# Optimization experiments

Measured on AMD Instinct MI355X. Metric: run time of the kernel, lower is better.

Reference implementation:

```python
import jax, jax.numpy as jnp
import numpy as np

V, S, D, H, L, F = 32000, 1024, 1024, 16, 6, 4096
DH = D // H          # 64
HALF = DH // 2       # 32
EPS = 1e-5
ROPE_BASE = 10000.0


def setup_inputs() -> dict:
    key = jax.random.key(0)
    ks = jax.random.split(key, 16)
    std = 0.02
    inp = {
        "tokens": jax.random.randint(ks[0], (4, S), 0, V),
        "tok_emb": jax.random.normal(ks[1], (V, D), jnp.float32) * std,
        "ln1_s": jnp.ones((L, D), jnp.float32),
        "ln1_b": jnp.zeros((L, D), jnp.float32),
        "w_qkv": jax.random.normal(ks[2], (L, D, 3 * D), jnp.float32) * std,
        "w_proj": jax.random.normal(ks[3], (L, D, D), jnp.float32) * std,
        "ln2_s": jnp.ones((L, D), jnp.float32),
        "ln2_b": jnp.zeros((L, D), jnp.float32),
        "w_in": jax.random.normal(ks[4], (L, D, 2 * F), jnp.float32) * std,
        "w_out": jax.random.normal(ks[5], (L, F, D), jnp.float32) * std,
        "lnf_s": jnp.ones((D,), jnp.float32),
        "lnf_b": jnp.zeros((D,), jnp.float32),
        "w_score": jax.random.normal(ks[6], (D, 1), jnp.float32) * std,
        "w_cls": jax.random.normal(ks[7], (D, S), jnp.float32) * std,
    }
    return inp


def _layernorm(x, s, b):
    m = x.mean(-1, keepdims=True)
    v = ((x - m) ** 2).mean(-1, keepdims=True)
    return (x - m) * jax.lax.rsqrt(v + EPS) * s + b


def _rotate_half(x):
    x_even = x[..., ::2]
    x_odd = x[..., 1::2]
    return jnp.stack((-x_odd, x_even), axis=-1).reshape(x.shape)


def _rope_tables():
    inv_freq = 1.0 / (ROPE_BASE ** (jnp.arange(0, DH, 2, dtype=jnp.float32) / DH))
    pos = jnp.arange(S, dtype=jnp.float32)
    freqs = jnp.outer(pos, inv_freq)               # [S, DH/2]
    cos = jnp.repeat(jnp.cos(freqs), 2, axis=-1)   # [S, DH]
    sin = jnp.repeat(jnp.sin(freqs), 2, axis=-1)
    return cos, sin


def _forward(tokens, tok_emb, ln1_s, ln1_b, w_qkv, w_proj, ln2_s, ln2_b,
             w_in, w_out, lnf_s, lnf_b, w_score, w_cls):
    B = tokens.shape[0]
    cos, sin = _rope_tables()                      # [S, DH], broadcast over B,H
    lower = jnp.tril(jnp.ones((S, S), jnp.bool_))  # j <= i -> "down" subspace
    scale = HALF ** -0.5

    h = tok_emb[tokens]                            # [B, S, D]

    def block(h, p):
        l1s, l1b, Wqkv, Wp, l2s, l2b, Wi, Wo = p
        # --- dual-triangle attention ---
        qkv = _layernorm(h, l1s, l1b) @ Wqkv       # [B, S, 3D]
        q, k, v = jnp.split(qkv, 3, axis=-1)
        def heads(t):
            return t.reshape(B, S, H, DH).transpose(0, 2, 1, 3)  # [B,H,S,DH]
        q, k, v = heads(q), heads(k), heads(v)
        q = q * cos + _rotate_half(q) * sin
        k = k * cos + _rotate_half(k) * sin
        a_up = jnp.einsum('bhqd,bhkd->bhqk', q[..., :HALF], k[..., :HALF]) * scale
        a_dn = jnp.einsum('bhqd,bhkd->bhqk', q[..., HALF:], k[..., HALF:]) * scale
        logits = jnp.where(lower, a_dn, a_up)
        w = jax.nn.softmax(logits, axis=-1)
        o = jnp.einsum('bhqk,bhkd->bhqd', w, v)
        o = o.transpose(0, 2, 1, 3).reshape(B, S, D) @ Wp
        h = h + o
        # --- SwiGLU MLP ---
        g = _layernorm(h, l2s, l2b) @ Wi           # [B, S, 2F]
        a, b = jnp.split(g, 2, axis=-1)
        h = h + (jax.nn.silu(a) * b) @ Wo
        return h, None

    h, _ = jax.lax.scan(block, h, (ln1_s, ln1_b, w_qkv, w_proj, ln2_s, ln2_b, w_in, w_out))

    # pooling head: per-position scores -> softmax over positions -> weighted sum
    h = _layernorm(h, lnf_s, lnf_b)
    scores = h @ w_score                           # [B, S, 1]
    pw = jax.nn.softmax(scores, axis=1)
    pooled = jnp.sum(pw * h, axis=1)               # [B, D]
    return pooled @ w_cls                          # [B, S] logits over positions


def reference(tokens, tok_emb, ln1_s, ln1_b, w_qkv, w_proj, ln2_s, ln2_b,
              w_in, w_out, lnf_s, lnf_b, w_score, w_cls):
    return _forward(tokens, tok_emb, ln1_s, ln1_b, w_qkv, w_proj, ln2_s, ln2_b,
                    w_in, w_out, lnf_s, lnf_b, w_score, w_cls)
```

## Files before the change

### kernel.cpp

```cpp
#include <hip/hip_runtime.h>

#define Bsz 4
#define Ssz 1024
#define Dsz 1024
#define Hn  16
#define DHn 64
#define Ln  6
#define Fsz 4096
#define SCALE_ 0.1767766952966369f
#define LOG2E_ 1.4426950408889634f

typedef unsigned long long u64;
typedef __attribute__((ext_vector_type(8))) short bf16x8;
typedef __attribute__((ext_vector_type(4))) float f32x4;

__device__ __forceinline__ unsigned short f2bf(float f) {
  union { float f; unsigned int u; } v; v.f = f;
  unsigned int u = v.u + 0x7fffu + ((v.u >> 16) & 1u);
  return (unsigned short)(u >> 16);
}
__device__ __forceinline__ float bf2f(unsigned short h) {
  union { unsigned int u; float f; } v; v.u = ((unsigned int)h) << 16;
  return v.f;
}
__device__ __forceinline__ void gload_lds16(const void* g, void* lds) {
  __builtin_amdgcn_global_load_lds(
      (const __attribute__((address_space(1))) unsigned int*)g,
      (__attribute__((address_space(3))) unsigned int*)lds, 16, 0, 0);
}

__device__ __forceinline__ int swz_addr(int r, int lq) {
  int line = r >> 1;
  int u = ((r & 1) << 2) | lq;
  int s = u ^ (line & 7);
  return line * 128 + s * 16;
}

__global__ __launch_bounds__(256) void k_cossin(float* __restrict__ cosT, float* __restrict__ sinT) {
  int idx = blockIdx.x * 256 + threadIdx.x;
  if (idx >= Ssz * 32) return;
  int s = idx >> 5, i = idx & 31;
  float inv = powf(10000.f, -((float)(2 * i)) / 64.f);
  float f = (float)s * inv;
  cosT[idx] = cosf(f);
  sinT[idx] = sinf(f);
}

__global__ __launch_bounds__(256) void k_embed(const int* __restrict__ tokens,
                                               const float* __restrict__ emb,
                                               float* __restrict__ h) {
  int rs = blockIdx.x;
  int t = threadIdx.x;
  int tok = tokens[rs];
  *(float4*)&h[(u64)rs * Dsz + t * 4] = *(const float4*)&emb[(u64)tok * Dsz + t * 4];
}

template <int BF16OUT>
__global__ __launch_bounds__(256) void k_layernorm(const float* __restrict__ x,
                                                   const float* __restrict__ sc,
                                                   const float* __restrict__ bi,
                                                   void* outv) {
  int row = blockIdx.x, t = threadIdx.x;
  const float* xr = x + (u64)row * Dsz;
  float4 v = *(const float4*)&xr[t * 4];
  float sm = v.x + v.y + v.z + v.w;
  float sq = v.x * v.x + v.y * v.y + v.z * v.z + v.w * v.w;
#pragma unroll
  for (int m = 1; m < 64; m <<= 1) { sm += __shfl_xor(sm, m); sq += __shfl_xor(sq, m); }
  __shared__ float r1[4], r2[4];
  if ((t & 63) == 0) { r1[t >> 6] = sm; r2[t >> 6] = sq; }
  __syncthreads();
  sm = r1[0] + r1[1] + r1[2] + r1[3];
  sq = r2[0] + r2[1] + r2[2] + r2[3];
  float mean = sm * (1.f / Dsz);
  float inv = rsqrtf(sq * (1.f / Dsz) - mean * mean + 1e-5f);
  float4 s4 = *(const float4*)&sc[t * 4];
  float4 b4 = *(const float4*)&bi[t * 4];
  float y0 = (v.x - mean) * inv * s4.x + b4.x;
  float y1 = (v.y - mean) * inv * s4.y + b4.y;
  float y2 = (v.z - mean) * inv * s4.z + b4.z;
  float y3 = (v.w - mean) * inv * s4.w + b4.w;
  if (BF16OUT) {
    ushort4 o; o.x = f2bf(y0); o.y = f2bf(y1); o.z = f2bf(y2); o.w = f2bf(y3);
    *(ushort4*)((unsigned short*)outv + (u64)row * Dsz + t * 4) = o;
  } else {
    float4 o; o.x = y0; o.y = y1; o.z = y2; o.w = y3;
    *(float4*)((float*)outv + (u64)row * Dsz + t * 4) = o;
  }
}

__global__ __launch_bounds__(256) void k_wt(const float* __restrict__ in,
                                            unsigned short* __restrict__ out, int K, int N) {
  in += (u64)blockIdx.z * K * N;
  out += (u64)blockIdx.z * K * N;
  __shared__ float tile[32][33];
  int nb = blockIdx.x * 32, kb = blockIdx.y * 32;
  int t = threadIdx.x;
  int r = t >> 3, c4 = (t & 7) * 4;
  float4 v = *(const float4*)&in[(u64)(kb + r) * N + nb + c4];
  tile[r][c4] = v.x; tile[r][c4 + 1] = v.y; tile[r][c4 + 2] = v.z; tile[r][c4 + 3] = v.w;
  __syncthreads();
  ushort4 o;
  o.x = f2bf(tile[c4][r]); o.y = f2bf(tile[c4 + 1][r]);
  o.z = f2bf(tile[c4 + 2][r]); o.w = f2bf(tile[c4 + 3][r]);
  *(ushort4*)&out[(u64)(nb + r) * K + kb + c4] = o;
}

__global__ __launch_bounds__(256) void k_wt_pair(const float* __restrict__ in,
                                                 unsigned short* __restrict__ out) {
  in += (u64)blockIdx.z * Dsz * 2 * Fsz;
  out += (u64)blockIdx.z * 2 * Fsz * Dsz;
  __shared__ float tile[32][33];
  int nb = blockIdx.x * 32, kb = blockIdx.y * 32;
  int t = threadIdx.x;
  int r = t >> 3, c4 = (t & 7) * 4;
  int s0 = nb >> 1;
  int srccol = (c4 < 16) ? (s0 + c4) : (Fsz + s0 + (c4 - 16));
  float4 v = *(const float4*)&in[(u64)(kb + r) * (2 * Fsz) + srccol];
  tile[r][c4] = v.x; tile[r][c4 + 1] = v.y; tile[r][c4 + 2] = v.z; tile[r][c4 + 3] = v.w;
  __syncthreads();
  int sc = (r >> 1) + (r & 1) * 16;
  ushort4 o;
  o.x = f2bf(tile[c4][sc]); o.y = f2bf(tile[c4 + 1][sc]);
  o.z = f2bf(tile[c4 + 2][sc]); o.w = f2bf(tile[c4 + 3][sc]);
  *(ushort4*)&out[(u64)(nb + r) * Dsz + kb + c4] = o;
}

template <int EPI>
__global__ __launch_bounds__(256, 3)
void k_ring(const unsigned short* __restrict__ A,
            const unsigned short* __restrict__ Bt,
            const float* resid, void* Cout,
            int M, int N, int K, int KH) {
  __shared__ char lds[3][16384] __attribute__((aligned(16)));
  int t = threadIdx.x, w = t >> 6, l = t & 63;
  int wm = w >> 1, wn = w & 1;
  int lr = l & 15, lq = l >> 4;
  int bn = blockIdx.x, bm = blockIdx.y, kz = blockIdx.z;
  int NT = KH >> 5;
  int g0 = t, g1 = t + 256;
  int L0 = g0 >> 3, u0 = (g0 & 7) ^ (L0 & 7), row0 = 2 * L0 + (u0 >> 2), kc0 = (u0 & 3) * 8;
  int L1 = g1 >> 3, u1 = (g1 & 7) ^ (L1 & 7), row1 = 2 * L1 + (u1 >> 2), kc1 = (u1 & 3) * 8;
  const unsigned short* Az = A + (u64)kz * KH;
  const unsigned short* Bz = Bt + (u64)kz * KH;
  const char* Asrc0 = (const char*)(Az + (u64)(bm * 128 + row0) * K + kc0);
  const char* Asrc1 = (const char*)(Az + (u64)(bm * 128 + row1) * K + kc1);
  const char* Bsrc0 = (const char*)(Bz + (u64)(bn * 128 + row0) * K + kc0);
  const char* Bsrc1 = (const char*)(Bz + (u64)(bn * 128 + row1) * K + kc1);
  f32x4 acc[4][4];
#pragma unroll
  for (int i = 0; i < 4; ++i)
#pragma unroll
    for (int j = 0; j < 4; ++j) acc[i][j] = (f32x4){0.f, 0.f, 0.f, 0.f};
#define STG(slot, jj) { char* d_ = lds[slot]; \
    gload_lds16(Asrc0 + (u64)(jj) * 64, d_ + g0 * 16); \
    gload_lds16(Asrc1 + (u64)(jj) * 64, d_ + g1 * 16); \
    gload_lds16(Bsrc0 + (u64)(jj) * 64, d_ + 8192 + g0 * 16); \
    gload_lds16(Bsrc1 + (u64)(jj) * 64, d_ + 8192 + g1 * 16); }
  STG(0, 0); STG(1, 1);
  int cs = 0, ss = 2;
  for (int j = 0; j < NT; ++j) {
    if (j < NT - 1) asm volatile("s_waitcnt vmcnt(4)" ::: "memory");
    else            asm volatile("s_waitcnt vmcnt(0)" ::: "memory");
    __builtin_amdgcn_s_barrier();
    __builtin_amdgcn_sched_barrier(0);
    const char* Ab = lds[cs];
    const char* Bb = lds[cs] + 8192;
    if (j + 2 < NT) STG(ss, j + 2);
    bf16x8 afrag[4], bfrag[4];
#pragma unroll
    for (int ni = 0; ni < 4; ++ni)
      bfrag[ni] = *(const bf16x8*)(Bb + swz_addr(wn * 64 + ni * 16 + lr, lq));
#pragma unroll
    for (int mi = 0; mi < 4; ++mi)
      afrag[mi] = *(const bf16x8*)(Ab + swz_addr(wm * 64 + mi * 16 + lr, lq));
    __builtin_amdgcn_s_setprio(1);
#pragma unroll
    for (int mi = 0; mi < 4; ++mi)
#pragma unroll
      for (int ni = 0; ni < 4; ++ni)
        acc[mi][ni] = __builtin_amdgcn_mfma_f32_16x16x32_bf16(afrag[mi], bfrag[ni], acc[mi][ni], 0, 0, 0);
    __builtin_amdgcn_s_setprio(0);
    cs = (cs == 2) ? 0 : cs + 1;
    ss = (ss == 2) ? 0 : ss + 1;
  }
#undef STG
  u64 zoff = (u64)kz * M * N;
#pragma unroll
  for (int mi = 0; mi < 4; ++mi)
#pragma unroll
    for (int ni = 0; ni < 4; ++ni)
#pragma unroll
      for (int r = 0; r < 4; ++r) {
        int row = bm * 128 + wm * 64 + mi * 16 + lq * 4 + r;
        int col = bn * 128 + wn * 64 + ni * 16 + lr;
        float v = acc[mi][ni][r];
        if (EPI == 3) {
          float pv = __shfl_xor(v, 1);
          if ((lr & 1) == 0) {
            float res = v / (1.f + __expf(-v)) * pv;
            ((unsigned short*)Cout)[(u64)row * (N >> 1) + (col >> 1)] = f2bf(res);
          }
        } else {
          u64 idx = (u64)row * N + col;
          if (EPI == 0) ((float*)Cout)[zoff + idx] = v;
          else if (EPI == 1) ((unsigned short*)Cout)[idx] = f2bf(v);
          else ((float*)Cout)[idx] = resid[idx] + v;
        }
      }
}

__global__ __launch_bounds__(256) void k_redres(const float* __restrict__ p0,
                                                const float* __restrict__ p1,
                                                float* __restrict__ h) {
  u64 i = ((u64)blockIdx.x * 256 + threadIdx.x) * 4;
  float4 a = *(float4*)&h[i];
  float4 b = *(const float4*)&p0[i];
  float4 c = *(const float4*)&p1[i];
  a.x += b.x + c.x; a.y += b.y + c.y; a.z += b.z + c.z; a.w += b.w + c.w;
  *(float4*)&h[i] = a;
}

__global__ __launch_bounds__(256) void k_rope_heads(const unsigned short* __restrict__ qkv,
                                                    const float* __restrict__ cosT,
                                                    const float* __restrict__ sinT,
                                                    unsigned short* __restrict__ q_r,
                                                    unsigned short* __restrict__ k_r,
                                                    unsigned short* __restrict__ v_t) {
  int st = blockIdx.x, hh = blockIdx.y, b = blockIdx.z;
  int t = threadIdx.x;
  int r = t >> 2, cg = (t & 3) * 16;
  int s = st * 64 + r;
  u64 rowb = ((u64)(b * Ssz + s)) * (3 * Dsz);
  u64 bh = (u64)(b * Hn + hh);
  const unsigned int* qp = (const unsigned int*)(qkv + rowb + hh * 64 + cg);
  const unsigned int* kp = (const unsigned int*)(qkv + rowb + Dsz + hh * 64 + cg);
  const unsigned short* vp = qkv + rowb + 2 * Dsz + hh * 64 + cg;
  uint4 qv0 = *(const uint4*)qp, qv1 = *(const uint4*)(qp + 4);
  uint4 kv0 = *(const uint4*)kp, kv1 = *(const uint4*)(kp + 4);
  int i0 = s * 32 + (cg >> 1);
  float4 cA0 = *(const float4*)&cosT[i0], cA1 = *(const float4*)&cosT[i0 + 4];
  float4 sA0 = *(const float4*)&sinT[i0], sA1 = *(const float4*)&sinT[i0 + 4];
  unsigned int qw[8] = {qv0.x, qv0.y, qv0.z, qv0.w, qv1.x, qv1.y, qv1.z, qv1.w};
  unsigned int kw[8] = {kv0.x, kv0.y, kv0.z, kv0.w, kv1.x, kv1.y, kv1.z, kv1.w};
  float cA[8] = {cA0.x, cA0.y, cA0.z, cA0.w, cA1.x, cA1.y, cA1.z, cA1.w};
  float sA[8] = {sA0.x, sA0.y, sA0.z, sA0.w, sA1.x, sA1.y, sA1.z, sA1.w};
  unsigned int oq[8], ok[8];
#pragma unroll
  for (int j = 0; j < 8; ++j) {
    float c = cA[j], sn = sA[j];
    float qe = bf2f((unsigned short)(qw[j] & 0xffff)), qo = bf2f((unsigned short)(qw[j] >> 16));
    float ke = bf2f((unsigned short)(kw[j] & 0xffff)), ko = bf2f((unsigned short)(kw[j] >> 16));
    oq[j] = (unsigned int)f2bf(qe * c - qo * sn) | ((unsigned int)f2bf(qo * c + qe * sn) << 16);
    ok[j] = (unsigned int)f2bf(ke * c - ko * sn) | ((unsigned int)f2bf(ko * c + ke * sn) << 16);
  }
  u64 dst = (bh * Ssz + s) * 64 + cg;
  uint4 a0; a0.x = oq[0]; a0.y = oq[1]; a0.z = oq[2]; a0.w = oq[3];
  uint4 a1; a1.x = oq[4]; a1.y = oq[5]; a1.z = oq[6]; a1.w = oq[7];
  ((uint4*)&q_r[dst])[0] = a0; ((uint4*)&q_r[dst])[1] = a1;
  uint4 b0; b0.x = ok[0]; b0.y = ok[1]; b0.z = ok[2]; b0.w = ok[3];
  uint4 b1; b1.x = ok[4]; b1.y = ok[5]; b1.z = ok[6]; b1.w = ok[7];
  ((uint4*)&k_r[dst])[0] = b0; ((uint4*)&k_r[dst])[1] = b1;
  __shared__ unsigned short vt_lds[64][65];
  uint4 vv0 = *(const uint4*)vp, vv1 = *(const uint4*)(vp + 8);
  unsigned int vw[8] = {vv0.x, vv0.y, vv0.z, vv0.w, vv1.x, vv1.y, vv1.z, vv1.w};
#pragma unroll
  for (int j = 0; j < 8; ++j) {
    vt_lds[r][cg + 2 * j] = (unsigned short)(vw[j] & 0xffff);
    vt_lds[r][cg + 2 * j + 1] = (unsigned short)(vw[j] >> 16);
  }
  __syncthreads();
  unsigned int ov[8];
#pragma unroll
  for (int j = 0; j < 8; ++j) {
    unsigned short lo = vt_lds[cg + 2 * j][r], hi = vt_lds[cg + 2 * j + 1][r];
    ov[j] = (unsigned int)lo | ((unsigned int)hi << 16);
  }
  u64 vdst = bh * ((u64)DHn * Ssz) + (u64)r * Ssz + st * 64 + cg;
  uint4 c0v; c0v.x = ov[0]; c0v.y = ov[1]; c0v.z = ov[2]; c0v.w = ov[3];
  uint4 c1v; c1v.x = ov[4]; c1v.y = ov[5]; c1v.z = ov[6]; c1v.w = ov[7];
  ((uint4*)&v_t[vdst])[0] = c0v; ((uint4*)&v_t[vdst])[1] = c1v;
}

__global__ __launch_bounds__(256) void k_attn(const unsigned short* __restrict__ qr,
                                              const unsigned short* __restrict__ kr,
                                              const unsigned short* __restrict__ vt,
                                              unsigned short* __restrict__ outp) {
  __shared__ unsigned short Klds[2][2][64 * 32] __attribute__((aligned(16)));
  __shared__ unsigned short Vlds[2][2][64 * 32] __attribute__((aligned(16)));
  __shared__ unsigned short Plds[4][16 * 64] __attribute__((aligned(16)));
  int qt = blockIdx.x, hh = blockIdx.y, b = blockIdx.z;
  int t = threadIdx.x, w = t >> 6, l = t & 63;
  int lr = l & 15, lq = l >> 4;
  u64 bh = (u64)(b * Hn + hh);
  const unsigned short* Qp = qr + bh * (Ssz * DHn);
  const unsigned short* Kp = kr + bh * (Ssz * DHn);
  const unsigned short* Vp = vt + bh * ((u64)DHn * Ssz);
  int q0 = qt * 64 + w * 16;
  bf16x8 qlo = *(const bf16x8*)&Qp[(q0 + lr) * DHn + lq * 8];
  bf16x8 qhi = *(const bf16x8*)&Qp[(q0 + lr) * DHn + 32 + lq * 8];
  int srow = t >> 2;
  int scol8 = (t & 3) * 8;
#define STAGEKV(bufi, kbase)                                                         \
  do {                                                                               \
    gload_lds16(&Kp[((kbase) + srow) * 64 + scol8],      (char*)&Klds[bufi][0][0] + t * 16); \
    gload_lds16(&Kp[((kbase) + srow) * 64 + 32 + scol8], (char*)&Klds[bufi][1][0] + t * 16); \
    gload_lds16(&Vp[(u64)srow * Ssz + (kbase) + scol8],      (char*)&Vlds[bufi][0][0] + t * 16); \
    gload_lds16(&Vp[(u64)srow * Ssz + (kbase) + 32 + scol8], (char*)&Vlds[bufi][1][0] + t * 16); \
  } while (0)
  float m_col = -1e30f, lsum = 0.f;
  float m_row[4] = {-1e30f, -1e30f, -1e30f, -1e30f};
  f32x4 o[4];
#pragma unroll
  for (int r = 0; r < 4; ++r) o[r] = (f32x4){0.f, 0.f, 0.f, 0.f};
  char* Pw = (char*)&Plds[w][0];

  STAGEKV(0, 0);
  asm volatile("s_waitcnt vmcnt(0)" ::: "memory");
  __syncthreads();
  int buf = 0;
  const float lsc = SCALE_ * LOG2E_;
  for (int kb = 0; kb < Ssz; kb += 64) {
    if (kb + 64 < Ssz) STAGEKV(buf ^ 1, kb + 64);
    float p[4][4];
#pragma unroll
    for (int ct = 0; ct < 4; ++ct) {
      bf16x8 klo = *(const bf16x8*)&Klds[buf][0][(ct * 16 + lr) * 32 + lq * 8];
      bf16x8 khi = *(const bf16x8*)&Klds[buf][1][(ct * 16 + lr) * 32 + lq * 8];
      f32x4 z = (f32x4){0.f, 0.f, 0.f, 0.f};
      f32x4 slo = __builtin_amdgcn_mfma_f32_16x16x32_bf16(klo, qlo, z, 0, 0, 0);
      f32x4 shi = __builtin_amdgcn_mfma_f32_16x16x32_bf16(khi, qhi, z, 0, 0, 0);
      int kg0 = kb + ct * 16 + lq * 4;
      int qg = q0 + lr;
#pragma unroll
      for (int r = 0; r < 4; ++r) p[ct][r] = (kg0 + r <= qg ? shi[r] : slo[r]) * lsc;
    }
    float tm = p[0][0];
#pragma unroll
    for (int ct = 0; ct < 4; ++ct)
#pragma unroll
      for (int r = 0; r < 4; ++r) tm = fmaxf(tm, p[ct][r]);
    tm = fmaxf(tm, __shfl_xor(tm, 16));
    tm = fmaxf(tm, __shfl_xor(tm, 32));
    if (__any(tm > m_col)) {
      float m_new = fmaxf(m_col, tm);
      lsum *= exp2f(m_col - m_new);
      m_col = m_new;
#pragma unroll
      for (int r = 0; r < 4; ++r) {
        float mr = __shfl(m_col, lq * 4 + r);
        float scf = exp2f(m_row[r] - mr);
        m_row[r] = mr;
        o[0][r] *= scf; o[1][r] *= scf; o[2][r] *= scf; o[3][r] *= scf;
      }
    }
#pragma unroll
    for (int ct = 0; ct < 4; ++ct) {
      float e0 = exp2f(p[ct][0] - m_col);
      float e1 = exp2f(p[ct][1] - m_col);
      float e2 = exp2f(p[ct][2] - m_col);
      float e3 = exp2f(p[ct][3] - m_col);
      lsum += e0 + e1 + e2 + e3;
      ushort4 pk; pk.x = f2bf(e0); pk.y = f2bf(e1); pk.z = f2bf(e2); pk.w = f2bf(e3);
      int byte_ = (lr * 128 + ct * 32 + lq * 8) ^ ((lr & 7) << 4);
      *(ushort4*)(Pw + byte_) = pk;
    }
    asm volatile("s_waitcnt lgkmcnt(0)" ::: "memory");
    __builtin_amdgcn_sched_barrier(0);
#pragma unroll
    for (int ks = 0; ks < 2; ++ks) {
      int pb = (lr * 128 + ks * 64 + lq * 16) ^ ((lr & 7) << 4);
      bf16x8 pa = *(const bf16x8*)(Pw + pb);
#pragma unroll
      for (int nt = 0; nt < 4; ++nt) {
        bf16x8 vb = *(const bf16x8*)&Vlds[buf][ks][(nt * 16 + lr) * 32 + lq * 8];
        o[nt] = __builtin_amdgcn_mfma_f32_16x16x32_bf16(pa, vb, o[nt], 0, 0, 0);
      }
    }
    asm volatile("s_waitcnt vmcnt(0)" ::: "memory");
    __syncthreads();
    buf ^= 1;
  }
  lsum += __shfl_xor(lsum, 16);
  lsum += __shfl_xor(lsum, 32);
  u64 obase = ((u64)b * Ssz) * Dsz + (u64)hh * DHn;
#pragma unroll
  for (int r = 0; r < 4; ++r) {
    float ls = __shfl(lsum, lq * 4 + r);
    float inv = 1.f / ls;
    int qrow = q0 + lq * 4 + r;
#pragma unroll
    for (int nt = 0; nt < 4; ++nt)
      outp[obase + (u64)qrow * Dsz + nt * 16 + lr] = f2bf(o[nt][r] * inv);
  }
#undef STAGEKV
}

__global__ __launch_bounds__(256) void k_scores(const float* __restrict__ hf,
                                                const float* __restrict__ wsc,
                                                float* __restrict__ scores) {
  int row = blockIdx.x * 4 + (threadIdx.x >> 6);
  int l = threadIdx.x & 63;
  const float* xr = hf + (u64)row * Dsz;
  float acc = 0.f;
#pragma unroll
  for (int j = 0; j < 4; ++j) {
    float4 v = *(const float4*)&xr[(j * 64 + l) * 4];
    float4 ww = *(const float4*)&wsc[(j * 64 + l) * 4];
    acc += v.x * ww.x + v.y * ww.y + v.z * ww.z + v.w * ww.w;
  }
#pragma unroll
  for (int m = 1; m < 64; m <<= 1) acc += __shfl_xor(acc, m);
  if (l == 0) scores[row] = acc;
}

__global__ __launch_bounds__(256) void k_softmax_s(const float* __restrict__ sc,
                                                   float* __restrict__ pw) {
  int b = blockIdx.x, t = threadIdx.x;
  const float* sr = sc + b * Ssz;
  float4 v = *(const float4*)&sr[t * 4];
  float mx = fmaxf(fmaxf(v.x, v.y), fmaxf(v.z, v.w));
#pragma unroll
  for (int m = 1; m < 64; m <<= 1) mx = fmaxf(mx, __shfl_xor(mx, m));
  __shared__ float red[4];
  if ((t & 63) == 0) red[t >> 6] = mx;
  __syncthreads();
  mx = fmaxf(fmaxf(red[0], red[1]), fmaxf(red[2], red[3]));
  float e0 = __expf(v.x - mx), e1 = __expf(v.y - mx), e2 = __expf(v.z - mx), e3 = __expf(v.w - mx);
  float sm = e0 + e1 + e2 + e3;
#pragma unroll
  for (int m = 1; m < 64; m <<= 1) sm += __shfl_xor(sm, m);
  __shared__ float red2[4];
  if ((t & 63) == 0) red2[t >> 6] = sm;
  __syncthreads();
  sm = red2[0] + red2[1] + red2[2] + red2[3];
  float inv = 1.f / sm;
  float4 o; o.x = e0 * inv; o.y = e1 * inv; o.z = e2 * inv; o.w = e3 * inv;
  *(float4*)&pw[b * Ssz + t * 4] = o;
}

__global__ __launch_bounds__(256) void k_pool1(const float* __restrict__ hf,
                                               const float* __restrict__ pw,
                                               float* __restrict__ part) {
  int d = blockIdx.x * 256 + threadIdx.x;
  int b = blockIdx.y, scn = blockIdx.z;
  const float* pwb = pw + b * Ssz + scn * 64;
  const float* hb = hf + ((u64)(b * Ssz + scn * 64)) * Dsz + d;
  float acc = 0.f;
#pragma unroll 4
  for (int s = 0; s < 64; ++s) acc += pwb[s] * hb[(u64)s * Dsz];
  part[(u64)(b * 16 + scn) * Dsz + d] = acc;
}
__global__ __launch_bounds__(256) void k_pool2(const float* __restrict__ part,
                                               float* __restrict__ pooled) {
  int d = blockIdx.x * 256 + threadIdx.x;
  int b = blockIdx.y;
  float acc = 0.f;
#pragma unroll
  for (int i = 0; i < 16; ++i) acc += part[(u64)(b * 16 + i) * Dsz + d];
  pooled[b * Dsz + d] = acc;
}

__global__ __launch_bounds__(256) void k_cls1(const float* __restrict__ pooled,
                                              const float* __restrict__ wcls,
                                              float* __restrict__ part) {
  int n = blockIdx.x * 64 + (threadIdx.x & 63);
  int b = threadIdx.x >> 6;
  int kz = blockIdx.y;
  const float* pb = pooled + b * Dsz + kz * 128;
  const float* wb = wcls + (u64)(kz * 128) * Ssz + n;
  float acc = 0.f;
#pragma unroll 4
  for (int k = 0; k < 128; ++k) acc += pb[k] * wb[(u64)k * Ssz];
  part[(u64)(kz * 4 + b) * Ssz + n] = acc;
}
__global__ __launch_bounds__(256) void k_cls2(const float* __restrict__ part,
                                              float* __restrict__ outp) {
  int n = blockIdx.x * 64 + (threadIdx.x & 63);
  int b = threadIdx.x >> 6;
  float acc = 0.f;
#pragma unroll
  for (int kz = 0; kz < 8; ++kz) acc += part[(u64)(kz * 4 + b) * Ssz + n];
  outp[b * Ssz + n] = acc;
}

extern "C" void kernel_launch(void* const* d_in, const int* in_sizes, int n_in,
                              void* d_out, int out_size, void* d_ws, size_t ws_size,
                              hipStream_t stream) {
  (void)in_sizes; (void)n_in; (void)out_size; (void)ws_size;
  const int*   tokens  = (const int*)  d_in[0];
  const float* tok_emb = (const float*)d_in[1];
  const float* ln1_s   = (const float*)d_in[2];
  const float* ln1_b   = (const float*)d_in[3];
  const float* w_qkv   = (const float*)d_in[4];
  const float* w_proj  = (const float*)d_in[5];
  const float* ln2_s   = (const float*)d_in[6];
  const float* ln2_b   = (const float*)d_in[7];
  const float* w_in    = (const float*)d_in[8];
  const float* w_out   = (const float*)d_in[9];
  const float* lnf_s   = (const float*)d_in[10];
  const float* lnf_b   = (const float*)d_in[11];
  const float* w_score = (const float*)d_in[12];
  const float* w_cls   = (const float*)d_in[13];
  float* outp = (float*)d_out;
  char* ws = (char*)d_ws;

  unsigned short* qkv    = (unsigned short*)(ws + 0);
  unsigned short* q_r    = (unsigned short*)(ws + 25165824ull);
  unsigned short* k_r    = (unsigned short*)(ws + 33554432ull);
  unsigned short* v_t    = (unsigned short*)(ws + 41943040ull);
  unsigned short* a_out  = (unsigned short*)(ws + 50331648ull);
  float*          hf     = (float*)(ws + 0);
  unsigned short* x_ln   = (unsigned short*)(ws + 67108864ull);
  unsigned short* mbuf   = (unsigned short*)(ws + 75497472ull);
  float*          h      = (float*)(ws + 109051904ull);
  float* cosT    = (float*)(ws + 125829120ull);
  float* sinT    = (float*)(ws + 125960192ull);
  float* scoresb = (float*)(ws + 126091264ull);
  float* pwb     = (float*)(ws + 126107648ull);
  float* pooledb = (float*)(ws + 126124032ull);
  float* poolpart= (float*)(ws + 126140416ull);
  float* clspart = (float*)(ws + 126402560ull);
  unsigned short* wqkv_t = (unsigned short*)(ws + 134217728ull);
  unsigned short* wproj_t= (unsigned short*)(ws + 171966464ull);
  unsigned short* win_t  = (unsigned short*)(ws + 184549376ull);
  unsigned short* wout_t = (unsigned short*)(ws + 285212672ull);
  float* skpart  = (float*)(ws + 335544320ull);

  dim3 blk(256);
  k_cossin<<<dim3(128), blk, 0, stream>>>(cosT, sinT);
  k_embed<<<dim3(4096), blk, 0, stream>>>(tokens, tok_emb, h);
  k_wt<<<dim3(96, 32, 6), blk, 0, stream>>>(w_qkv, wqkv_t, Dsz, 3 * Dsz);
  k_wt<<<dim3(32, 32, 6), blk, 0, stream>>>(w_proj, wproj_t, Dsz, Dsz);
  k_wt_pair<<<dim3(256, 32, 6), blk, 0, stream>>>(w_in, win_t);
  k_wt<<<dim3(32, 128, 6), blk, 0, stream>>>(w_out, wout_t, Fsz, Dsz);

  for (int l = 0; l < Ln; ++l) {
    unsigned short* wq = wqkv_t + (u64)l * 3145728ull;
    unsigned short* wp = wproj_t + (u64)l * 1048576ull;
    unsigned short* wi = win_t + (u64)l * 8388608ull;
    unsigned short* wo = wout_t + (u64)l * 4194304ull;
    k_layernorm<1><<<dim3(4096), blk, 0, stream>>>(h, ln1_s + l * Dsz, ln1_b + l * Dsz, (void*)x_ln);
    k_ring<1><<<dim3(24, 32), blk, 0, stream>>>(x_ln, wq, nullptr, (void*)qkv, 4096, 3072, 1024, 1024);
    k_rope_heads<<<dim3(16, 16, 4), blk, 0, stream>>>(qkv, cosT, sinT, q_r, k_r, v_t);
    k_attn<<<dim3(16, 16, 4), blk, 0, stream>>>(q_r, k_r, v_t, a_out);
    k_ring<2><<<dim3(8, 32), blk, 0, stream>>>(a_out, wp, h, (void*)h, 4096, 1024, 1024, 1024);
    k_layernorm<1><<<dim3(4096), blk, 0, stream>>>(h, ln2_s + l * Dsz, ln2_b + l * Dsz, (void*)x_ln);
    k_ring<3><<<dim3(64, 32), blk, 0, stream>>>(x_ln, wi, nullptr, (void*)mbuf, 4096, 8192, 1024, 1024);
    k_ring<0><<<dim3(8, 32, 2), blk, 0, stream>>>(mbuf, wo, nullptr, (void*)skpart, 4096, 1024, 4096, 2048);
    k_redres<<<dim3(4096), blk, 0, stream>>>(skpart, skpart + 4194304ull, h);
  }

  k_layernorm<0><<<dim3(4096), blk, 0, stream>>>(h, lnf_s, lnf_b, (void*)hf);
  k_scores<<<dim3(1024), blk, 0, stream>>>(hf, w_score, scoresb);
  k_softmax_s<<<dim3(4), blk, 0, stream>>>(scoresb, pwb);
  k_pool1<<<dim3(4, 4, 16), blk, 0, stream>>>(hf, pwb, poolpart);
  k_pool2<<<dim3(4, 4), blk, 0, stream>>>(poolpart, pooledb);
  k_cls1<<<dim3(16, 8), blk, 0, stream>>>(pooledb, w_cls, clspart);
  k_cls2<<<dim3(16), blk, 0, stream>>>(clspart, outp);
}
```

Before: 1.970 ms.

## Fuse RoPE/head scatter into QKV GEMM, residual into LN, skip masked attention MFMAs

The QKV GEMM epilogue now applies RoPE and scatters q/k into head-major layout and v into transposed layout, which removes the separate rope kernel and the qkv round-trip through memory. The split-K residual reduction is fused with the next layer's first layernorm. In attention, tiles entirely below or above the diagonal compute only the one MFMA they need instead of both. The risk is that the GEMM epilogue now does scattered 2-byte stores, especially the transposed v writes, which are poorly coalesced.

Measured after the change: 1.963 ms. About the same (-0.4%).

```diff
diff --git a/kernel.cpp b/kernel.cpp
--- a/kernel.cpp
+++ b/kernel.cpp
@@ -89,6 +89,51 @@
   }
 }
 
+__global__ __launch_bounds__(256) void k_redres_ln(const float* __restrict__ p0,
+                                                   const float* __restrict__ p1,
+                                                   float* __restrict__ h,
+                                                   const float* __restrict__ sc,
+                                                   const float* __restrict__ bi,
+                                                   unsigned short* __restrict__ xo) {
+  int row = blockIdx.x, t = threadIdx.x;
+  u64 base = (u64)row * Dsz + t * 4;
+  float4 a = *(float4*)&h[base];
+  float4 b0 = *(const float4*)&p0[base];
+  float4 c0 = *(const float4*)&p1[base];
+  a.x += b0.x + c0.x; a.y += b0.y + c0.y; a.z += b0.z + c0.z; a.w += b0.w + c0.w;
+  *(float4*)&h[base] = a;
+  float sm = a.x + a.y + a.z + a.w;
+  float sq = a.x * a.x + a.y * a.y + a.z * a.z + a.w * a.w;
+#pragma unroll
+  for (int m = 1; m < 64; m <<= 1) { sm += __shfl_xor(sm, m); sq += __shfl_xor(sq, m); }
+  __shared__ float r1[4], r2[4];
+  if ((t & 63) == 0) { r1[t >> 6] = sm; r2[t >> 6] = sq; }
+  __syncthreads();
+  sm = r1[0] + r1[1] + r1[2] + r1[3];
+  sq = r2[0] + r2[1] + r2[2] + r2[3];
+  float mean = sm * (1.f / Dsz);
+  float inv = rsqrtf(sq * (1.f / Dsz) - mean * mean + 1e-5f);
+  float4 s4 = *(const float4*)&sc[t * 4];
+  float4 b4 = *(const float4*)&bi[t * 4];
+  ushort4 o;
+  o.x = f2bf((a.x - mean) * inv * s4.x + b4.x);
+  o.y = f2bf((a.y - mean) * inv * s4.y + b4.y);
+  o.z = f2bf((a.z - mean) * inv * s4.z + b4.z);
+  o.w = f2bf((a.w - mean) * inv * s4.w + b4.w);
+  *(ushort4*)&xo[base] = o;
+}
+
+__global__ __launch_bounds__(256) void k_redres(const float* __restrict__ p0,
+                                                const float* __restrict__ p1,
+                                                float* __restrict__ h) {
+  u64 i = ((u64)blockIdx.x * 256 + threadIdx.x) * 4;
+  float4 a = *(float4*)&h[i];
+  float4 b = *(const float4*)&p0[i];
+  float4 c = *(const float4*)&p1[i];
+  a.x += b.x + c.x; a.y += b.y + c.y; a.z += b.z + c.z; a.w += b.w + c.w;
+  *(float4*)&h[i] = a;
+}
+
 __global__ __launch_bounds__(256) void k_wt(const float* __restrict__ in,
                                             unsigned short* __restrict__ out, int K, int N) {
   in += (u64)blockIdx.z * K * N;
@@ -131,7 +176,9 @@
 void k_ring(const unsigned short* __restrict__ A,
             const unsigned short* __restrict__ Bt,
             const float* resid, void* Cout,
-            int M, int N, int K, int KH) {
+            int M, int N, int K, int KH,
+            unsigned short* qr, unsigned short* kr, unsigned short* vt,
+            const float* cosT, const float* sinT) {
   __shared__ char lds[3][16384] __attribute__((aligned(16)));
   int t = threadIdx.x, w = t >> 6, l = t & 63;
   int wm = w >> 1, wn = w & 1;
@@ -201,6 +248,19 @@
             float res = v / (1.f + __expf(-v)) * pv;
             ((unsigned short*)Cout)[(u64)row * (N >> 1) + (col >> 1)] = f2bf(res);
           }
+        } else if (EPI == 4) {
+          float pv = __shfl_xor(v, 1);
+          int b = row >> 10, s = row & 1023;
+          int sec = col >> 10, c = col & 1023, hh = c >> 6, dh = c & 63;
+          if (sec == 2) {
+            vt[((u64)(b * Hn + hh) * DHn + dh) * Ssz + s] = f2bf(v);
+          } else {
+            int ci = s * 32 + (dh >> 1);
+            float cs_ = cosT[ci], sn_ = sinT[ci];
+            float out = (dh & 1) ? (v * cs_ + pv * sn_) : (v * cs_ - pv * sn_);
+            u64 dst = ((u64)(b * Hn + hh) * Ssz + s) * DHn + dh;
+            (sec == 0 ? qr : kr)[dst] = f2bf(out);
+          }
         } else {
           u64 idx = (u64)row * N + col;
           if (EPI == 0) ((float*)Cout)[zoff + idx] = v;
@@ -208,78 +268,6 @@
           else ((float*)Cout)[idx] = resid[idx] + v;
         }
       }
-}
-
-__global__ __launch_bounds__(256) void k_redres(const float* __restrict__ p0,
-                                                const float* __restrict__ p1,
-                                                float* __restrict__ h) {
-  u64 i = ((u64)blockIdx.x * 256 + threadIdx.x) * 4;
-  float4 a = *(float4*)&h[i];
-  float4 b = *(const float4*)&p0[i];
-  float4 c = *(const float4*)&p1[i];
-  a.x += b.x + c.x; a.y += b.y + c.y; a.z += b.z + c.z; a.w += b.w + c.w;
-  *(float4*)&h[i] = a;
-}
-
-__global__ __launch_bounds__(256) void k_rope_heads(const unsigned short* __restrict__ qkv,
-                                                    const float* __restrict__ cosT,
-                                                    const float* __restrict__ sinT,
-                                                    unsigned short* __restrict__ q_r,
-                                                    unsigned short* __restrict__ k_r,
-                                                    unsigned short* __restrict__ v_t) {
-  int st = blockIdx.x, hh = blockIdx.y, b = blockIdx.z;
-  int t = threadIdx.x;
-  int r = t >> 2, cg = (t & 3) * 16;
-  int s = st * 64 + r;
-  u64 rowb = ((u64)(b * Ssz + s)) * (3 * Dsz);
-  u64 bh = (u64)(b * Hn + hh);
-  const unsigned int* qp = (const unsigned int*)(qkv + rowb + hh * 64 + cg);
-  const unsigned int* kp = (const unsigned int*)(qkv + rowb + Dsz + hh * 64 + cg);
-  const unsigned short* vp = qkv + rowb + 2 * Dsz + hh * 64 + cg;
-  uint4 qv0 = *(const uint4*)qp, qv1 = *(const uint4*)(qp + 4);
-  uint4 kv0 = *(const uint4*)kp, kv1 = *(const uint4*)(kp + 4);
-  int i0 = s * 32 + (cg >> 1);
-  float4 cA0 = *(const float4*)&cosT[i0], cA1 = *(const float4*)&cosT[i0 + 4];
-  float4 sA0 = *(const float4*)&sinT[i0], sA1 = *(const float4*)&sinT[i0 + 4];
-  unsigned int qw[8] = {qv0.x, qv0.y, qv0.z, qv0.w, qv1.x, qv1.y, qv1.z, qv1.w};
-  unsigned int kw[8] = {kv0.x, kv0.y, kv0.z, kv0.w, kv1.x, kv1.y, kv1.z, kv1.w};
-  float cA[8] = {cA0.x, cA0.y, cA0.z, cA0.w, cA1.x, cA1.y, cA1.z, cA1.w};
-  float sA[8] = {sA0.x, sA0.y, sA0.z, sA0.w, sA1.x, sA1.y, sA1.z, sA1.w};
-  unsigned int oq[8], ok[8];
-#pragma unroll
-  for (int j = 0; j < 8; ++j) {
-    float c = cA[j], sn = sA[j];
-    float qe = bf2f((unsigned short)(qw[j] & 0xffff)), qo = bf2f((unsigned short)(qw[j] >> 16));
-    float ke = bf2f((unsigned short)(kw[j] & 0xffff)), ko = bf2f((unsigned short)(kw[j] >> 16));
-    oq[j] = (unsigned int)f2bf(qe * c - qo * sn) | ((unsigned int)f2bf(qo * c + qe * sn) << 16);
-    ok[j] = (unsigned int)f2bf(ke * c - ko * sn) | ((unsigned int)f2bf(ko * c + ke * sn) << 16);
-  }
-  u64 dst = (bh * Ssz + s) * 64 + cg;
-  uint4 a0; a0.x = oq[0]; a0.y = oq[1]; a0.z = oq[2]; a0.w = oq[3];
-  uint4 a1; a1.x = oq[4]; a1.y = oq[5]; a1.z = oq[6]; a1.w = oq[7];
-  ((uint4*)&q_r[dst])[0] = a0; ((uint4*)&q_r[dst])[1] = a1;
-  uint4 b0; b0.x = ok[0]; b0.y = ok[1]; b0.z = ok[2]; b0.w = ok[3];
-  uint4 b1; b1.x = ok[4]; b1.y = ok[5]; b1.z = ok[6]; b1.w = ok[7];
-  ((uint4*)&k_r[dst])[0] = b0; ((uint4*)&k_r[dst])[1] = b1;
-  __shared__ unsigned short vt_lds[64][65];
-  uint4 vv0 = *(const uint4*)vp, vv1 = *(const uint4*)(vp + 8);
-  unsigned int vw[8] = {vv0.x, vv0.y, vv0.z, vv0.w, vv1.x, vv1.y, vv1.z, vv1.w};
-#pragma unroll
-  for (int j = 0; j < 8; ++j) {
-    vt_lds[r][cg + 2 * j] = (unsigned short)(vw[j] & 0xffff);
-    vt_lds[r][cg + 2 * j + 1] = (unsigned short)(vw[j] >> 16);
-  }
-  __syncthreads();
-  unsigned int ov[8];
-#pragma unroll
-  for (int j = 0; j < 8; ++j) {
-    unsigned short lo = vt_lds[cg + 2 * j][r], hi = vt_lds[cg + 2 * j + 1][r];
-    ov[j] = (unsigned int)lo | ((unsigned int)hi << 16);
-  }
-  u64 vdst = bh * ((u64)DHn * Ssz) + (u64)r * Ssz + st * 64 + cg;
-  uint4 c0v; c0v.x = ov[0]; c0v.y = ov[1]; c0v.z = ov[2]; c0v.w = ov[3];
-  uint4 c1v; c1v.x = ov[4]; c1v.y = ov[5]; c1v.z = ov[6]; c1v.w = ov[7];
-  ((uint4*)&v_t[vdst])[0] = c0v; ((uint4*)&v_t[vdst])[1] = c1v;
 }
 
 __global__ __launch_bounds__(256) void k_attn(const unsigned short* __restrict__ qr,
@@ -325,15 +313,28 @@
     float p[4][4];
 #pragma unroll
     for (int ct = 0; ct < 4; ++ct) {
-      bf16x8 klo = *(const bf16x8*)&Klds[buf][0][(ct * 16 + lr) * 32 + lq * 8];
-      bf16x8 khi = *(const bf16x8*)&Klds[buf][1][(ct * 16 + lr) * 32 + lq * 8];
+      int kc = kb + ct * 16;
       f32x4 z = (f32x4){0.f, 0.f, 0.f, 0.f};
-      f32x4 slo = __builtin_amdgcn_mfma_f32_16x16x32_bf16(klo, qlo, z, 0, 0, 0);
-      f32x4 shi = __builtin_amdgcn_mfma_f32_16x16x32_bf16(khi, qhi, z, 0, 0, 0);
-      int kg0 = kb + ct * 16 + lq * 4;
-      int qg = q0 + lr;
-#pragma unroll
-      for (int r = 0; r < 4; ++r) p[ct][r] = (kg0 + r <= qg ? shi[r] : slo[r]) * lsc;
+      if (kc < q0) {
+        bf16x8 khi = *(const bf16x8*)&Klds[buf][1][(ct * 16 + lr) * 32 + lq * 8];
+        f32x4 shi = __builtin_amdgcn_mfma_f32_16x16x32_bf16(khi, qhi, z, 0, 0, 0);
+#pragma unroll
+        for (int r = 0; r < 4; ++r) p[ct][r] = shi[r] * lsc;
+      } else if (kc > q0) {
+        bf16x8 klo = *(const bf16x8*)&Klds[buf][0][(ct * 16 + lr) * 32 + lq * 8];
+        f32x4 slo = __builtin_amdgcn_mfma_f32_16x16x32_bf16(klo, qlo, z, 0, 0, 0);
+#pragma unroll
+        for (int r = 0; r < 4; ++r) p[ct][r] = slo[r] * lsc;
+      } else {
+        bf16x8 klo = *(const bf16x8*)&Klds[buf][0][(ct * 16 + lr) * 32 + lq * 8];
+        bf16x8 khi = *(const bf16x8*)&Klds[buf][1][(ct * 16 + lr) * 32 + lq * 8];
+        f32x4 slo = __builtin_amdgcn_mfma_f32_16x16x32_bf16(klo, qlo, z, 0, 0, 0);
+        f32x4 shi = __builtin_amdgcn_mfma_f32_16x16x32_bf16(khi, qhi, z, 0, 0, 0);
+        int kg0 = kc + lq * 4;
+        int qg = q0 + lr;
+#pragma unroll
+        for (int r = 0; r < 4; ++r) p[ct][r] = (kg0 + r <= qg ? shi[r] : slo[r]) * lsc;
+      }
     }
     float tm = p[0][0];
 #pragma unroll
@@ -505,7 +506,6 @@
   float* outp = (float*)d_out;
   char* ws = (char*)d_ws;
 
-  unsigned short* qkv    = (unsigned short*)(ws + 0);
   unsigned short* q_r    = (unsigned short*)(ws + 25165824ull);
   unsigned short* k_r    = (unsigned short*)(ws + 33554432ull);
   unsigned short* v_t    = (unsigned short*)(ws + 41943040ull);
@@ -535,20 +535,27 @@
   k_wt_pair<<<dim3(256, 32, 6), blk, 0, stream>>>(w_in, win_t);
   k_wt<<<dim3(32, 128, 6), blk, 0, stream>>>(w_out, wout_t, Fsz, Dsz);
 
+  k_layernorm<1><<<dim3(4096), blk, 0, stream>>>(h, ln1_s, ln1_b, (void*)x_ln);
   for (int l = 0; l < Ln; ++l) {
     unsigned short* wq = wqkv_t + (u64)l * 3145728ull;
     unsigned short* wp = wproj_t + (u64)l * 1048576ull;
     unsigned short* wi = win_t + (u64)l * 8388608ull;
     unsigned short* wo = wout_t + (u64)l * 4194304ull;
-    k_layernorm<1><<<dim3(4096), blk, 0, stream>>>(h, ln1_s + l * Dsz, ln1_b + l * Dsz, (void*)x_ln);
-    k_ring<1><<<dim3(24, 32), blk, 0, stream>>>(x_ln, wq, nullptr, (void*)qkv, 4096, 3072, 1024, 1024);
-    k_rope_heads<<<dim3(16, 16, 4), blk, 0, stream>>>(qkv, cosT, sinT, q_r, k_r, v_t);
+    k_ring<4><<<dim3(24, 32), blk, 0, stream>>>(x_ln, wq, nullptr, nullptr,
+        4096, 3072, 1024, 1024, q_r, k_r, v_t, cosT, sinT);
     k_attn<<<dim3(16, 16, 4), blk, 0, stream>>>(q_r, k_r, v_t, a_out);
-    k_ring<2><<<dim3(8, 32), blk, 0, stream>>>(a_out, wp, h, (void*)h, 4096, 1024, 1024, 1024);
+    k_ring<2><<<dim3(8, 32), blk, 0, stream>>>(a_out, wp, h, (void*)h,
+        4096, 1024, 1024, 1024, nullptr, nullptr, nullptr, nullptr, nullptr);
     k_layernorm<1><<<dim3(4096), blk, 0, stream>>>(h, ln2_s + l * Dsz, ln2_b + l * Dsz, (void*)x_ln);
-    k_ring<3><<<dim3(64, 32), blk, 0, stream>>>(x_ln, wi, nullptr, (void*)mbuf, 4096, 8192, 1024, 1024);
-    k_ring<0><<<dim3(8, 32, 2), blk, 0, stream>>>(mbuf, wo, nullptr, (void*)skpart, 4096, 1024, 4096, 2048);
-    k_redres<<<dim3(4096), blk, 0, stream>>>(skpart, skpart + 4194304ull, h);
+    k_ring<3><<<dim3(64, 32), blk, 0, stream>>>(x_ln, wi, nullptr, (void*)mbuf,
+        4096, 8192, 1024, 1024, nullptr, nullptr, nullptr, nullptr, nullptr);
+    k_ring<0><<<dim3(8, 32, 2), blk, 0, stream>>>(mbuf, wo, nullptr, (void*)skpart,
+        4096, 1024, 4096, 2048, nullptr, nullptr, nullptr, nullptr, nullptr);
+    if (l < Ln - 1)
+      k_redres_ln<<<dim3(4096), blk, 0, stream>>>(skpart, skpart + 4194304ull, h,
+          ln1_s + (l + 1) * Dsz, ln1_b + (l + 1) * Dsz, x_ln);
+    else
+      k_redres<<<dim3(4096), blk, 0, stream>>>(skpart, skpart + 4194304ull, h);
   }
 
   k_layernorm<0><<<dim3(4096), blk, 0, stream>>>(h, lnf_s, lnf_b, (void*)hf);
```
